# Kernel optimization log

Measured on AMD Instinct MI355X. Metric: run time of the kernel, lower is better.

Reference implementation:

```python
import jax, jax.numpy as jnp
import numpy as np

N, E, E_LBL = 50000, 800000, 200000
D_IN, H = 128, 128


def setup_inputs() -> dict:
    key = jax.random.key(0)
    ks = jax.random.split(key, 12)
    s = 0.05
    return {
        "x": jax.random.normal(ks[0], (N, D_IN), jnp.float32),
        "edge_index": jax.random.randint(ks[1], (2, E), 0, N, jnp.int64),
        "edge_label_index": jax.random.randint(ks[2], (2, E_LBL), 0, N, jnp.int64),
        "pre_w": jax.random.normal(ks[3], (D_IN, H), jnp.float32) * s,
        "pre_b": jax.random.normal(ks[4], (H,), jnp.float32) * s,
        "Wx": jax.random.normal(ks[5], (3, 2, H, H), jnp.float32) * s,  # gates z,r,h x cheb orders T0,T1
        "bx": jax.random.normal(ks[6], (3, H), jnp.float32) * s,
        "Wh": jax.random.normal(ks[7], (3, 2, H, H), jnp.float32) * s,
        "bh": jax.random.normal(ks[8], (3, H), jnp.float32) * s,
        "post_w": jax.random.normal(ks[9], (H, 2), jnp.float32) * s,
        "post_b": jax.random.normal(ks[10], (2,), jnp.float32) * s,
    }


def reference(x, edge_index, edge_label_index, pre_w, pre_b, Wx, bx, Wh, bh, post_w, post_b):
    n = x.shape[0]
    src, dst = edge_index[0], edge_index[1]

    # Scaled Chebyshev Laplacian (sym norm, lambda_max=2): L_hat = -D^{-1/2} A D^{-1/2}
    # (diagonal of L_hat is exactly 0, so only off-diagonal edge terms remain).
    deg = jax.ops.segment_sum(jnp.ones_like(src, dtype=x.dtype), src, num_segments=n)
    dinv = jnp.where(deg > 0, jax.lax.rsqrt(jnp.maximum(deg, 1.0)), 0.0)
    w = -(dinv[src] * dinv[dst])  # [E]

    def lap(v):  # L_hat @ v : gather src rows, weight, scatter-add at dst
        return jax.ops.segment_sum(w[:, None] * v[src], dst, num_segments=n)

    def cheb(v, Lv, W2, b):  # ChebConv K=2: T0(v)@W0 + T1(v)@W1 + b
        return v @ W2[0] + Lv @ W2[1] + b

    # pre: Linear(input_dim -> hidden)
    Xh = x @ pre_w + pre_b  # [N, H]
    LX = lap(Xh)

    # GConvGRU single step, H0 = 0
    Hc = jnp.zeros_like(Xh)
    LH = lap(Hc)
    Z = jax.nn.sigmoid(cheb(Xh, LX, Wx[0], bx[0]) + cheb(Hc, LH, Wh[0], bh[0]))
    R = jax.nn.sigmoid(cheb(Xh, LX, Wx[1], bx[1]) + cheb(Hc, LH, Wh[1], bh[1]))
    HR = Hc * R
    LHR = lap(HR)
    Ht = jnp.tanh(cheb(Xh, LX, Wx[2], bx[2]) + cheb(HR, LHR, Wh[2], bh[2]))
    Hc = Z * Hc + (1.0 - Z) * Ht

    h = jax.nn.relu(Hc)
    # link decoder: gather endpoints, hadamard, Linear(H->2), sum over logits
    hprod = h[edge_label_index[0]] * h[edge_label_index[1]]  # [E_lbl, H]
    out = hprod @ post_w + post_b  # [E_lbl, 2]
    return jnp.sum(out, axis=-1)  # [E_lbl]
```

## Files before the change

kernel.cpp:

```cpp
#include <hip/hip_runtime.h>
#include <math.h>


#define RND 2048
#define SORT_CAP 1536
#define CAPB 6144

typedef __attribute__((ext_vector_type(4))) float f32x4;
typedef __attribute__((ext_vector_type(8))) short short8;
typedef __attribute__((ext_vector_type(4))) unsigned u32x4;

static __device__ __forceinline__ unsigned short f2b(float f) {
  union { float f; unsigned u; } v; v.f = f;
  unsigned r = (v.u + 0x7fffu + ((v.u >> 16) & 1u)) >> 16;
  return (unsigned short)r;
}
static __device__ __forceinline__ float b2f(unsigned short s) {
  union { unsigned u; float f; } v; v.u = ((unsigned)s) << 16;
  return v.f;
}

__global__ __launch_bounds__(256) void prep_kernel(const float* __restrict__ pre_w, const float* __restrict__ Wx,
                                                   const float* __restrict__ bx, const float* __restrict__ bh,
                                                   const float* __restrict__ post_w, const float* __restrict__ post_b,
                                                   unsigned short* __restrict__ Bt1c, unsigned short* __restrict__ Btc2,
                                                   float* __restrict__ fb2, float* __restrict__ pwsum,
                                                   int* __restrict__ binPos) {
  int e = blockIdx.x * 256 + threadIdx.x;
  if (e < 512) binPos[e] = (e & 255) * CAPB;
  if (e < 16384) {
    int kc = e >> 12, r = e & 4095, col = r >> 5, kk = r & 31;
    Bt1c[e] = f2b(pre_w[(kc * 32 + kk) * 128 + col]);
  }
  int e2 = e - 16384;
  if (e2 >= 0 && e2 < 65536) {
    int kc = e2 >> 13, r = e2 & 8191, cB = r >> 5, kk = r & 31;
    int k = kc * 32 + kk, half = k >> 7, ki = k & 127;
    int cb = cB >> 7, r7 = cB & 127, nw6 = r7 >> 6, u2 = r7 & 63;
    int g = (u2 >= 32) ? 2 : 0, hcol = cb * 64 + nw6 * 32 + (u2 & 31);
    Btc2[e2] = f2b(Wx[((g * 2 + half) * 128 + ki) * 128 + hcol]);
  }
  int e3 = e - (16384 + 65536);
  if (e3 >= 0 && e3 < 256) {
    int cB = e3;
    int cb = cB >> 7, r7 = cB & 127, nw6 = r7 >> 6, u2 = r7 & 63;
    int g = (u2 >= 32) ? 2 : 0, hcol = cb * 64 + nw6 * 32 + (u2 & 31);
    fb2[cB] = bx[g * 128 + hcol] + bh[g * 128 + hcol];
  }
  int e4 = e - (16384 + 65536 + 256);
  if (e4 >= 0 && e4 < 128) pwsum[e4] = post_w[2 * e4] + post_w[2 * e4 + 1];
  if (e4 == 128) pwsum[128] = post_b[0] + post_b[1];
}

union SMemU {
  struct { unsigned short As[128 * 40]; unsigned short Bs[128 * 40]; } g;
  struct { unsigned ent[RND]; int hist[256], lstart[256], lofs[256], gbase[256], wsum[4];
           unsigned char ebin[RND], sb[RND]; } s;
};

__global__ __launch_bounds__(256) void mega1_kernel(const float* __restrict__ x,
                                                    const unsigned short* __restrict__ Bt1c,
                                                    const float* __restrict__ pre_b,
                                                    unsigned short* __restrict__ Xq,
                                                    const int* __restrict__ ei, int* __restrict__ binPos,
                                                    unsigned* __restrict__ bins,
                                                    unsigned char* __restrict__ sbins,
                                                    int N, int E, int RB) {
  __shared__ SMemU sm;
  const int t = threadIdx.x;

  if ((int)blockIdx.x < RB) {
    unsigned short* As = sm.g.As;
    unsigned short* Bs = sm.g.Bs;
    const int r0 = blockIdx.x * 128;
    const int w = t >> 6, lane = t & 63;
    const int m = lane & 15, q = lane >> 4;
    const int mw = (w >> 1) * 64, nw = (w & 1) * 64;

    f32x4 acc[4][4];
#pragma unroll
    for (int i = 0; i < 4; ++i)
#pragma unroll
      for (int j = 0; j < 4; ++j) acc[i][j] = {0.f, 0.f, 0.f, 0.f};

    const int arow = t >> 1, aseg = t & 1;
    const bool arow_ok = (r0 + arow) < N;
    const float* asrc0 = &x[(size_t)(r0 + arow) * 128 + aseg * 16];

    float4 cav[4]; short8 cbv0, cbv1;
    {
      if (arow_ok) {
#pragma unroll
        for (int i = 0; i < 4; ++i) cav[i] = *(const float4*)(asrc0 + i * 4);
      } else {
#pragma unroll
        for (int i = 0; i < 4; ++i) cav[i] = make_float4(0.f, 0.f, 0.f, 0.f);
      }
      const char* src = (const char*)Bt1c + t * 32;
      cbv0 = *(const short8*)src;
      cbv1 = *(const short8*)(src + 16);
    }

    for (int kc = 0; kc < 4; ++kc) {
      __syncthreads();
      {
        short8 t0, t1;
#pragma unroll
        for (int i = 0; i < 2; ++i) {
          t0[i * 4 + 0] = (short)f2b(cav[i].x); t0[i * 4 + 1] = (short)f2b(cav[i].y);
          t0[i * 4 + 2] = (short)f2b(cav[i].z); t0[i * 4 + 3] = (short)f2b(cav[i].w);
          t1[i * 4 + 0] = (short)f2b(cav[i + 2].x); t1[i * 4 + 1] = (short)f2b(cav[i + 2].y);
          t1[i * 4 + 2] = (short)f2b(cav[i + 2].z); t1[i * 4 + 3] = (short)f2b(cav[i + 2].w);
        }
        *(short8*)&As[arow * 40 + aseg * 16] = t0;
        *(short8*)&As[arow * 40 + aseg * 16 + 8] = t1;
        int bcol = t >> 1, boff = (t & 1) * 16;
        *(short8*)&Bs[bcol * 40 + boff] = cbv0;
        *(short8*)&Bs[bcol * 40 + boff + 8] = cbv1;
      }
      float4 nav[4]; short8 nbv0, nbv1;
      if (kc < 3) {
        if (arow_ok) {
          const float* src = asrc0 + (kc + 1) * 32;
#pragma unroll
          for (int i = 0; i < 4; ++i) nav[i] = *(const float4*)(src + i * 4);
        } else {
#pragma unroll
          for (int i = 0; i < 4; ++i) nav[i] = make_float4(0.f, 0.f, 0.f, 0.f);
        }
        const char* src = (const char*)Bt1c + (size_t)(kc + 1) * 8192 + t * 32;
        nbv0 = *(const short8*)src;
        nbv1 = *(const short8*)(src + 16);
      }
      __syncthreads();
      short8 af[4], bf[4];
#pragma unroll
      for (int i = 0; i < 4; ++i) af[i] = *(const short8*)&As[(mw + i * 16 + m) * 40 + q * 8];
#pragma unroll
      for (int j = 0; j < 4; ++j) bf[j] = *(const short8*)&Bs[(nw + j * 16 + m) * 40 + q * 8];
#pragma unroll
      for (int i = 0; i < 4; ++i)
#pragma unroll
        for (int j = 0; j < 4; ++j)
          acc[i][j] = __builtin_amdgcn_mfma_f32_16x16x32_bf16(af[i], bf[j], acc[i][j], 0, 0, 0);
      if (kc < 3) {
#pragma unroll
        for (int i = 0; i < 4; ++i) cav[i] = nav[i];
        cbv0 = nbv0; cbv1 = nbv1;
      }
    }

#pragma unroll
    for (int i = 0; i < 4; ++i) {
      int rb2 = r0 + mw + i * 16 + q * 4;
#pragma unroll
      for (int j = 0; j < 4; ++j) {
        int col = nw + j * 16 + m;
        float bias = pre_b[col];
#pragma unroll
        for (int r = 0; r < 4; ++r) {
          int row = rb2 + r;
          if (row < N) Xq[(size_t)row * 128 + col] = f2b(acc[i][j][r] + bias);
        }
      }
    }
    return;
  }

  unsigned* ent = sm.s.ent;
  unsigned char* ebin = sm.s.ebin;
  unsigned char* sb = sm.s.sb;
  int* hist = sm.s.hist;
  int* lstart = sm.s.lstart;
  int* lofs = sm.s.lofs;
  int* gbase = sm.s.gbase;
  int* wsum = sm.s.wsum;
  const int sbid = (int)blockIdx.x - RB;
  const int snum = (int)gridDim.x - RB;
  const int w = t >> 6, lane = t & 63;
  for (long long base = (long long)sbid * RND; base < E; base += (long long)snum * RND) {
    int cnt = (int)(((long long)E - base < RND) ? (E - base) : RND);
    if (t < 256) hist[t] = 0;
    __syncthreads();
    int my_s[8], my_d[8];
#pragma unroll
    for (int u = 0; u < 8; ++u) {
      int i = u * 256 + t;
      my_s[u] = -1;
      if (i < cnt) {
        int idx = (int)base + i;
        my_s[u] = ei[idx];
        my_d[u] = ei[E + idx];
        atomicAdd(&hist[my_d[u] >> 8], 1);
      }
    }
    __syncthreads();
    {
      int h = hist[t];
      hist[t] = 0;
      int v = h;
#pragma unroll
      for (int dd = 1; dd < 64; dd <<= 1) { int uu = __shfl_up(v, dd); if (lane >= dd) v += uu; }
      if (lane == 63) wsum[w] = v;
      __syncthreads();
      int woff = 0;
#pragma unroll
      for (int ww = 0; ww < 3; ++ww) if (ww < w) woff += wsum[ww];
      int excl = v - h + woff;
      lstart[t] = excl; lofs[t] = excl;
      if (h > 0) gbase[t] = atomicAdd(&binPos[t], h);
    }
    __syncthreads();
#pragma unroll
    for (int u = 0; u < 8; ++u) {
      if (my_s[u] >= 0) {
        int b = my_d[u] >> 8;
        int p = atomicAdd(&lofs[b], 1);
        ent[p] = (unsigned)my_s[u] | ((unsigned)(my_d[u] & 255) << 16);
        ebin[p] = (unsigned char)b;
        atomicAdd(&hist[my_s[u] >> 8], 1);
      }
    }
    __syncthreads();
    for (int i = t; i < cnt; i += 256) {
      int b = ebin[i];
      int pos = gbase[b] + (i - lstart[b]);
      if (pos < (b + 1) * CAPB) bins[pos] = ent[i];
    }
    __syncthreads();
    {
      int h = hist[t];
      int v = h;
#pragma unroll
      for (int dd = 1; dd < 64; dd <<= 1) { int uu = __shfl_up(v, dd); if (lane >= dd) v += uu; }
      if (lane == 63) wsum[w] = v;
      __syncthreads();
      int woff = 0;
#pragma unroll
      for (int ww = 0; ww < 3; ++ww) if (ww < w) woff += wsum[ww];
      int excl = v - h + woff;
      lstart[t] = excl; lofs[t] = excl;
      if (h > 0) gbase[t] = atomicAdd(&binPos[256 + t], h);
    }
    __syncthreads();
#pragma unroll
    for (int u = 0; u < 8; ++u) {
      if (my_s[u] >= 0) {
        int b = my_s[u] >> 8;
        int p = atomicAdd(&lofs[b], 1);
        sb[p] = (unsigned char)(my_s[u] & 255);
        ebin[p] = (unsigned char)b;
      }
    }
    __syncthreads();
    for (int i = t; i < cnt; i += 256) {
      int b = ebin[i];
      int pos = gbase[b] + (i - lstart[b]);
      if (pos < (b + 1) * CAPB) sbins[pos] = sb[i];
    }
    __syncthreads();
  }
}

__global__ __launch_bounds__(512) void deghist_kernel(const unsigned char* __restrict__ sbins,
                                                      const int* __restrict__ binPos,
                                                      const unsigned short* __restrict__ Xq,
                                                      unsigned short* __restrict__ Xs,
                                                      float* __restrict__ dinvNeg, int N) {
  __shared__ int h[256];
  __shared__ float sdi[256];
  const int t = threadIdx.x;
  const int bin = blockIdx.x;
  if (t < 256) h[t] = 0;
  __syncthreads();
  int T2 = binPos[256 + bin] - bin * CAPB;
  if (T2 > CAPB) T2 = CAPB;
  const unsigned char* __restrict__ p = sbins + (size_t)bin * CAPB;
  for (int i = t; i < T2; i += 512) atomicAdd(&h[p[i]], 1);
  __syncthreads();
  if (t < 256) {
    int node = bin * 256 + t;
    float di = h[t] > 0 ? rsqrtf((float)h[t]) : 0.0f;
    sdi[t] = di;
    if (node < N) dinvNeg[node] = -di;
  }
  __syncthreads();
  const int wv = t >> 6, lane = t & 63;
  const int g4 = lane >> 4, sl = lane & 15;
#pragma unroll
  for (int it = 0; it < 8; ++it) {
    int r = wv * 32 + it * 4 + g4;
    int rnode = bin * 256 + r;
    if (rnode < N) {
      float di_r = sdi[r];
      u32x4 v = *(const u32x4*)((const char*)Xq + (size_t)rnode * 256 + sl * 16);
      u32x4 o;
#pragma unroll
      for (int k = 0; k < 4; ++k) {
        union { unsigned u32; float f; } fl, fh;
        fl.u32 = v[k] << 16; fh.u32 = v[k] & 0xffff0000u;
        o[k] = (unsigned)f2b(fl.f * di_r) | ((unsigned)f2b(fh.f * di_r) << 16);
      }
      *(u32x4*)((char*)Xs + (size_t)rnode * 256 + sl * 16) = o;
    }
  }
}

__global__ __launch_bounds__(512) void lap_bin_kernel(const unsigned short* __restrict__ Xs,
                                                      unsigned short* __restrict__ LXc,
                                                      const unsigned* __restrict__ bins,
                                                      const int* __restrict__ binPos,
                                                      const float* __restrict__ dinvNeg, int N) {
  __shared__ unsigned eLDS[CAPB];
  __shared__ unsigned short sortS[SORT_CAP];
  __shared__ int hist[64], start[64], off[64];
  const int t = threadIdx.x;
  const int bin = blockIdx.x >> 2, qt = blockIdx.x & 3;
  const int lo = bin * CAPB;
  int T = binPos[bin] - lo;
  if (T > CAPB) T = CAPB;
  const unsigned* __restrict__ ebase = &bins[lo];
  if (t < 64) hist[t] = 0;
  __syncthreads();
  for (int i = t; i < T; i += 512) {
    unsigned e = ebase[i];
    eLDS[i] = e;
    int dl = (e >> 16) & 255;
    if ((dl >> 6) == qt) atomicAdd(&hist[dl & 63], 1);
  }
  __syncthreads();
  if (t < 64) {
    int h = hist[t];
    int v = h;
#pragma unroll
    for (int d = 1; d < 64; d <<= 1) {
      int u = __shfl_up(v, d);
      if (t >= d) v += u;
    }
    start[t] = v - h;
    off[t] = v - h;
  }
  __syncthreads();
  for (int i = t; i < T; i += 512) {
    unsigned e = eLDS[i];
    int dl = (e >> 16) & 255;
    if ((dl >> 6) == qt) {
      int p = atomicAdd(&off[dl & 63], 1);
      if (p < SORT_CAP) sortS[p] = (unsigned short)(e & 0xFFFFu);
    }
  }
  __syncthreads();
  const int wv = t >> 6, lane = t & 63;
  const int g4 = lane >> 4, sl = lane & 15;
  for (int n = wv; n < 64; n += 8) {
    int node = bin * 256 + qt * 64 + n;
    if (node >= N) break;
    int st = start[n], cnum = hist[n];
    float acc[8] = {0.f, 0.f, 0.f, 0.f, 0.f, 0.f, 0.f, 0.f};
    for (int j = 0; j < cnum; j += 8) {
#pragma unroll
      for (int u = 0; u < 2; ++u) {
        int idx = j + u * 4 + g4;
        bool val = idx < cnum;
        int s = sortS[st + (val ? idx : 0)];
        u32x4 vv = *(const u32x4*)((const char*)Xs + (size_t)s * 256 + sl * 16);
        if (val) {
#pragma unroll
          for (int k = 0; k < 4; ++k) {
            union { unsigned u32; float f; } fl, fh;
            fl.u32 = vv[k] << 16; fh.u32 = vv[k] & 0xffff0000u;
            acc[2 * k] += fl.f;
            acc[2 * k + 1] += fh.f;
          }
        }
      }
    }
#pragma unroll
    for (int k = 0; k < 8; ++k) {
      acc[k] += __shfl_xor(acc[k], 16);
      acc[k] += __shfl_xor(acc[k], 32);
    }
    if (g4 == 0) {
      float wd = dinvNeg[node];
      u32x4 o;
#pragma unroll
      for (int k = 0; k < 4; ++k)
        o[k] = (unsigned)f2b(acc[2 * k] * wd) | ((unsigned)f2b(acc[2 * k + 1] * wd) << 16);
      *(u32x4*)((char*)LXc + (size_t)node * 256 + sl * 16) = o;
    }
  }
}

__global__ __launch_bounds__(256) void gemm2_mfma(const unsigned short* __restrict__ Xq,
                                                  const unsigned short* __restrict__ LXc,
                                                  const unsigned short* __restrict__ Btc2,
                                                  const float* __restrict__ fb2,
                                                  unsigned short* __restrict__ hb, int N) {
  __shared__ unsigned short As[128 * 40];
  __shared__ unsigned short Bs[128 * 40];
  const int t = threadIdx.x;
  const int rb = blockIdx.x >> 1, cb = blockIdx.x & 1;
  const int r0 = rb * 128;
  const int w = t >> 6, lane = t & 63;
  const int m = lane & 15, q = lane >> 4;
  const int mw = (w >> 1) * 64, nw = (w & 1) * 64;

  f32x4 acc[4][4];
#pragma unroll
  for (int i = 0; i < 4; ++i)
#pragma unroll
    for (int j = 0; j < 4; ++j) acc[i][j] = {0.f, 0.f, 0.f, 0.f};

  const int arow = t >> 1;
  const int aoff = (t & 1) * 32;
  const char* aXq = (const char*)Xq + (size_t)(r0 + arow) * 256 + aoff;
  const char* aLX = (const char*)LXc + (size_t)(r0 + arow) * 256 + aoff;
  const char* bsrc0 = (const char*)Btc2 + (size_t)cb * 8192 + t * 32;

  short8 cav0, cav1, cbv0, cbv1;
  cav0 = *(const short8*)aXq;
  cav1 = *(const short8*)(aXq + 16);
  cbv0 = *(const short8*)bsrc0;
  cbv1 = *(const short8*)(bsrc0 + 16);

  for (int kc = 0; kc < 8; ++kc) {
    __syncthreads();
    *(short8*)&As[arow * 40 + (aoff >> 1)] = cav0;
    *(short8*)&As[arow * 40 + (aoff >> 1) + 8] = cav1;
    {
      int bcol = t >> 1, boff = (t & 1) * 16;
      *(short8*)&Bs[bcol * 40 + boff] = cbv0;
      *(short8*)&Bs[bcol * 40 + boff + 8] = cbv1;
    }
    short8 nav0, nav1, nbv0, nbv1;
    if (kc < 7) {
      int kn = kc + 1;
      const char* asrc = (kn < 4) ? (aXq + kn * 64) : (aLX + (kn - 4) * 64);
      nav0 = *(const short8*)asrc;
      nav1 = *(const short8*)(asrc + 16);
      const char* bsrc = bsrc0 + (size_t)kn * 16384;
      nbv0 = *(const short8*)bsrc;
      nbv1 = *(const short8*)(bsrc + 16);
    }
    __syncthreads();
    short8 af[4], bf[4];
#pragma unroll
    for (int i = 0; i < 4; ++i) af[i] = *(const short8*)&As[(mw + i * 16 + m) * 40 + q * 8];
#pragma unroll
    for (int j = 0; j < 4; ++j) bf[j] = *(const short8*)&Bs[(nw + j * 16 + m) * 40 + q * 8];
#pragma unroll
    for (int i = 0; i < 4; ++i)
#pragma unroll
      for (int j = 0; j < 4; ++j)
        acc[i][j] = __builtin_amdgcn_mfma_f32_16x16x32_bf16(af[i], bf[j], acc[i][j], 0, 0, 0);
    if (kc < 7) { cav0 = nav0; cav1 = nav1; cbv0 = nbv0; cbv1 = nbv1; }
  }

#pragma unroll
  for (int i = 0; i < 4; ++i) {
    int rbase = r0 + mw + i * 16 + q * 4;
#pragma unroll
    for (int jz = 0; jz < 2; ++jz) {
      int cBz = cb * 128 + nw + jz * 16 + m;
      int hc = cb * 64 + (nw >> 1) + jz * 16 + m;
      float bz = fb2[cBz], bt = fb2[cBz + 32];
#pragma unroll
      for (int r = 0; r < 4; ++r) {
        int row = rbase + r;
        if (row < N) {
          float zp = acc[i][jz][r] + bz;
          float tp = acc[i][jz + 2][r] + bt;
          float zs = 1.0f / (1.0f + __expf(-zp));
          float th = tanhf(tp);
          hb[(size_t)row * 128 + hc] = f2b(fmaxf((1.0f - zs) * th, 0.0f));
        }
      }
    }
  }
}

__global__ __launch_bounds__(256) void decoder_kernel(const unsigned short* __restrict__ hb,
                                                      const int* __restrict__ eli,
                                                      const float* __restrict__ pwsum, float* __restrict__ out, int M) {
  int t = threadIdx.x;
  int i = blockIdx.x * 16 + (t >> 4);
  int l = t & 15;
  if (i >= M) return;
  int a = eli[i], b = eli[M + i];
  int k = l * 8;
  short8 va = *(const short8*)&hb[(size_t)a * 128 + k];
  short8 vb = *(const short8*)&hb[(size_t)b * 128 + k];
  const float4* pwp = (const float4*)&pwsum[k];
  float4 p0 = pwp[0], p1 = pwp[1];
  float s = 0.0f;
  s += b2f((unsigned short)va[0]) * b2f((unsigned short)vb[0]) * p0.x;
  s += b2f((unsigned short)va[1]) * b2f((unsigned short)vb[1]) * p0.y;
  s += b2f((unsigned short)va[2]) * b2f((unsigned short)vb[2]) * p0.z;
  s += b2f((unsigned short)va[3]) * b2f((unsigned short)vb[3]) * p0.w;
  s += b2f((unsigned short)va[4]) * b2f((unsigned short)vb[4]) * p1.x;
  s += b2f((unsigned short)va[5]) * b2f((unsigned short)vb[5]) * p1.y;
  s += b2f((unsigned short)va[6]) * b2f((unsigned short)vb[6]) * p1.z;
  s += b2f((unsigned short)va[7]) * b2f((unsigned short)vb[7]) * p1.w;
#pragma unroll
  for (int off = 8; off; off >>= 1) s += __shfl_xor(s, off);
  if (l == 0) out[i] = s + pwsum[128];
}

extern "C" void kernel_launch(void* const* d_in, const int* in_sizes, int n_in,
                              void* d_out, int out_size, void* d_ws, size_t ws_size,
                              hipStream_t stream) {
  const float* x      = (const float*)d_in[0];
  const int*   ei     = (const int*)d_in[1];
  const int*   eli    = (const int*)d_in[2];
  const float* pre_w  = (const float*)d_in[3];
  const float* pre_b  = (const float*)d_in[4];
  const float* Wx     = (const float*)d_in[5];
  const float* bx     = (const float*)d_in[6];
  const float* bh     = (const float*)d_in[8];
  const float* post_w = (const float*)d_in[9];
  const float* post_b = (const float*)d_in[10];
  float* out = (float*)d_out;

  const int N = in_sizes[0] / 128;
  const int E = in_sizes[1] / 2;
  const int M = in_sizes[2] / 2;
  const int RB = (N + 127) / 128;
  const int NBIN = (N + 255) / 256;
  const int SCAT = (E + RND - 1) / RND;

  char* W = (char*)d_ws;
  size_t o = 0;
  float* dinvNeg = (float*)(W + o); o += (size_t)N * 4;
  int* binPos = (int*)(W + o);    o += 2048;
  o = (o + 255) & ~(size_t)255;
  unsigned* bins = (unsigned*)(W + o); o += (size_t)NBIN * CAPB * 4;
  o = (o + 255) & ~(size_t)255;
  unsigned char* sbins = (unsigned char*)(W + o); o += (size_t)NBIN * CAPB;
  o = (o + 255) & ~(size_t)255;
  unsigned short* Xq = (unsigned short*)(W + o);  o += (size_t)RB * 128 * 256;
  unsigned short* Xs = (unsigned short*)(W + o);  o += (size_t)RB * 128 * 256;
  unsigned short* LXc = (unsigned short*)(W + o); o += (size_t)RB * 128 * 256;
  unsigned short* hb = (unsigned short*)(W + o);  o += (size_t)N * 256;
  unsigned short* Bt1c = (unsigned short*)(W + o); o += 32768;
  unsigned short* Btc2 = (unsigned short*)(W + o); o += 131072;
  float* fb2 = (float*)(W + o);  o += 1024;
  float* pwsum = (float*)(W + o); o += 768;

  prep_kernel<<<322, 256, 0, stream>>>(pre_w, Wx, bx, bh, post_w, post_b, Bt1c, Btc2, fb2, pwsum,
                                       binPos);
  mega1_kernel<<<RB + SCAT, 256, 0, stream>>>(x, Bt1c, pre_b, Xq, ei, binPos, bins, sbins, N, E, RB);
  deghist_kernel<<<NBIN, 512, 0, stream>>>(sbins, binPos, Xq, Xs, dinvNeg, N);
  lap_bin_kernel<<<NBIN * 4, 512, 0, stream>>>(Xs, LXc, bins, binPos, dinvNeg, N);
  gemm2_mfma<<<RB * 2, 256, 0, stream>>>(Xq, LXc, Btc2, fb2, hb, N);
  decoder_kernel<<<(M + 15) / 16, 256, 0, stream>>>(hb, eli, pwsum, out, M);
}
```

Baseline: 197.5 us.

## Store scaled features in FP8 E4M3 for Laplacian gather and pad bin counters

```diff
diff --git a/kernel.cpp b/kernel.cpp
--- a/kernel.cpp
+++ b/kernel.cpp
@@ -9,6 +9,7 @@
 typedef __attribute__((ext_vector_type(4))) float f32x4;
 typedef __attribute__((ext_vector_type(8))) short short8;
 typedef __attribute__((ext_vector_type(4))) unsigned u32x4;
+typedef __attribute__((ext_vector_type(2))) unsigned u32x2;
 
 static __device__ __forceinline__ unsigned short f2b(float f) {
   union { float f; unsigned u; } v; v.f = f;
@@ -18,6 +19,17 @@
 static __device__ __forceinline__ float b2f(unsigned short s) {
   union { unsigned u; float f; } v; v.u = ((unsigned)s) << 16;
   return v.f;
+}
+static __device__ __forceinline__ unsigned f2e4m3(float f) {
+  unsigned su = (__float_as_uint(f) >> 24) & 0x80u;
+  float a = fminf(fabsf(f), 448.0f) * 0x1.0p-120f;
+  unsigned u = __float_as_uint(a);
+  u += 0x7FFFFu + ((u >> 20) & 1u);
+  return su | ((u >> 20) & 0x7Fu);
+}
+static __device__ __forceinline__ float e4m32f(unsigned b) {
+  unsigned u = ((b & 0x80u) << 24) | ((b & 0x7Fu) << 20);
+  return __uint_as_float(u) * 0x1.0p120f;
 }
 
 __global__ __launch_bounds__(256) void prep_kernel(const float* __restrict__ pre_w, const float* __restrict__ Wx,
@@ -27,7 +39,7 @@
                                                    float* __restrict__ fb2, float* __restrict__ pwsum,
                                                    int* __restrict__ binPos) {
   int e = blockIdx.x * 256 + threadIdx.x;
-  if (e < 512) binPos[e] = (e & 255) * CAPB;
+  if (e < 512) binPos[e * 16] = (e & 255) * CAPB;
   if (e < 16384) {
     int kc = e >> 12, r = e & 4095, col = r >> 5, kk = r & 31;
     Bt1c[e] = f2b(pre_w[(kc * 32 + kk) * 128 + col]);
@@ -208,7 +220,7 @@
       for (int ww = 0; ww < 3; ++ww) if (ww < w) woff += wsum[ww];
       int excl = v - h + woff;
       lstart[t] = excl; lofs[t] = excl;
-      if (h > 0) gbase[t] = atomicAdd(&binPos[t], h);
+      if (h > 0) gbase[t] = atomicAdd(&binPos[t * 16], h);
     }
     __syncthreads();
 #pragma unroll
@@ -240,7 +252,7 @@
       for (int ww = 0; ww < 3; ++ww) if (ww < w) woff += wsum[ww];
       int excl = v - h + woff;
       lstart[t] = excl; lofs[t] = excl;
-      if (h > 0) gbase[t] = atomicAdd(&binPos[256 + t], h);
+      if (h > 0) gbase[t] = atomicAdd(&binPos[(256 + t) * 16], h);
     }
     __syncthreads();
 #pragma unroll
@@ -265,7 +277,7 @@
 __global__ __launch_bounds__(512) void deghist_kernel(const unsigned char* __restrict__ sbins,
                                                       const int* __restrict__ binPos,
                                                       const unsigned short* __restrict__ Xq,
-                                                      unsigned short* __restrict__ Xs,
+                                                      unsigned char* __restrict__ Xs,
                                                       float* __restrict__ dinvNeg, int N) {
   __shared__ int h[256];
   __shared__ float sdi[256];
@@ -273,7 +285,7 @@
   const int bin = blockIdx.x;
   if (t < 256) h[t] = 0;
   __syncthreads();
-  int T2 = binPos[256 + bin] - bin * CAPB;
+  int T2 = binPos[(256 + bin) * 16] - bin * CAPB;
   if (T2 > CAPB) T2 = CAPB;
   const unsigned char* __restrict__ p = sbins + (size_t)bin * CAPB;
   for (int i = t; i < T2; i += 512) atomicAdd(&h[p[i]], 1);
@@ -294,19 +306,26 @@
     if (rnode < N) {
       float di_r = sdi[r];
       u32x4 v = *(const u32x4*)((const char*)Xq + (size_t)rnode * 256 + sl * 16);
-      u32x4 o;
-#pragma unroll
-      for (int k = 0; k < 4; ++k) {
-        union { unsigned u32; float f; } fl, fh;
-        fl.u32 = v[k] << 16; fh.u32 = v[k] & 0xffff0000u;
-        o[k] = (unsigned)f2b(fl.f * di_r) | ((unsigned)f2b(fh.f * di_r) << 16);
-      }
-      *(u32x4*)((char*)Xs + (size_t)rnode * 256 + sl * 16) = o;
-    }
-  }
-}
-
-__global__ __launch_bounds__(512) void lap_bin_kernel(const unsigned short* __restrict__ Xs,
+      u32x2 o;
+#pragma unroll
+      for (int k = 0; k < 2; ++k) {
+        unsigned w0 = 0;
+#pragma unroll
+        for (int j = 0; j < 2; ++j) {
+          unsigned vv = v[k * 2 + j];
+          union { unsigned u32; float f; } fl, fh;
+          fl.u32 = vv << 16; fh.u32 = vv & 0xffff0000u;
+          w0 |= f2e4m3(fl.f * di_r) << (j * 16);
+          w0 |= f2e4m3(fh.f * di_r) << (j * 16 + 8);
+        }
+        o[k] = w0;
+      }
+      *(u32x2*)((char*)Xs + (size_t)rnode * 128 + sl * 8) = o;
+    }
+  }
+}
+
+__global__ __launch_bounds__(512) void lap_bin_kernel(const unsigned char* __restrict__ Xs,
                                                       unsigned short* __restrict__ LXc,
                                                       const unsigned* __restrict__ bins,
                                                       const int* __restrict__ binPos,
@@ -317,7 +336,7 @@
   const int t = threadIdx.x;
   const int bin = blockIdx.x >> 2, qt = blockIdx.x & 3;
   const int lo = bin * CAPB;
-  int T = binPos[bin] - lo;
+  int T = binPos[bin * 16] - lo;
   if (T > CAPB) T = CAPB;
   const unsigned* __restrict__ ebase = &bins[lo];
   if (t < 64) hist[t] = 0;
@@ -363,14 +382,15 @@
         int idx = j + u * 4 + g4;
         bool val = idx < cnum;
         int s = sortS[st + (val ? idx : 0)];
-        u32x4 vv = *(const u32x4*)((const char*)Xs + (size_t)s * 256 + sl * 16);
+        u32x2 vv = *(const u32x2*)((const char*)Xs + (size_t)s * 128 + sl * 8);
         if (val) {
 #pragma unroll
-          for (int k = 0; k < 4; ++k) {
-            union { unsigned u32; float f; } fl, fh;
-            fl.u32 = vv[k] << 16; fh.u32 = vv[k] & 0xffff0000u;
-            acc[2 * k] += fl.f;
-            acc[2 * k + 1] += fh.f;
+          for (int kk = 0; kk < 2; ++kk) {
+            unsigned wv2 = vv[kk];
+            acc[4 * kk + 0] += e4m32f(wv2 & 0xFFu);
+            acc[4 * kk + 1] += e4m32f((wv2 >> 8) & 0xFFu);
+            acc[4 * kk + 2] += e4m32f((wv2 >> 16) & 0xFFu);
+            acc[4 * kk + 3] += e4m32f(wv2 >> 24);
           }
         }
       }
@@ -531,14 +551,15 @@
   char* W = (char*)d_ws;
   size_t o = 0;
   float* dinvNeg = (float*)(W + o); o += (size_t)N * 4;
-  int* binPos = (int*)(W + o);    o += 2048;
+  o = (o + 255) & ~(size_t)255;
+  int* binPos = (int*)(W + o);    o += 512 * 16 * 4;
   o = (o + 255) & ~(size_t)255;
   unsigned* bins = (unsigned*)(W + o); o += (size_t)NBIN * CAPB * 4;
   o = (o + 255) & ~(size_t)255;
   unsigned char* sbins = (unsigned char*)(W + o); o += (size_t)NBIN * CAPB;
   o = (o + 255) & ~(size_t)255;
   unsigned short* Xq = (unsigned short*)(W + o);  o += (size_t)RB * 128 * 256;
-  unsigned short* Xs = (unsigned short*)(W + o);  o += (size_t)RB * 128 * 256;
+  unsigned char* Xs = (unsigned char*)(W + o);    o += (size_t)RB * 128 * 128;
   unsigned short* LXc = (unsigned short*)(W + o); o += (size_t)RB * 128 * 256;
   unsigned short* hb = (unsigned short*)(W + o);  o += (size_t)N * 256;
   unsigned short* Bt1c = (unsigned short*)(W + o); o += 32768;
```

After: 216.6 us. 1.1x slower.

## Pad bin counters, vectorize edge loads, pack bin id, split lap bins finer

Applied to the files above, without the earlier changes.

```diff
diff --git a/kernel.cpp b/kernel.cpp
--- a/kernel.cpp
+++ b/kernel.cpp
@@ -9,6 +9,7 @@
 typedef __attribute__((ext_vector_type(4))) float f32x4;
 typedef __attribute__((ext_vector_type(8))) short short8;
 typedef __attribute__((ext_vector_type(4))) unsigned u32x4;
+typedef __attribute__((ext_vector_type(4))) int i32x4;
 
 static __device__ __forceinline__ unsigned short f2b(float f) {
   union { float f; unsigned u; } v; v.f = f;
@@ -27,7 +28,7 @@
                                                    float* __restrict__ fb2, float* __restrict__ pwsum,
                                                    int* __restrict__ binPos) {
   int e = blockIdx.x * 256 + threadIdx.x;
-  if (e < 512) binPos[e] = (e & 255) * CAPB;
+  if (e < 512) binPos[e * 16] = (e & 255) * CAPB;
   if (e < 16384) {
     int kc = e >> 12, r = e & 4095, col = r >> 5, kk = r & 31;
     Bt1c[e] = f2b(pre_w[(kc * 32 + kk) * 128 + col]);
@@ -183,16 +184,27 @@
     if (t < 256) hist[t] = 0;
     __syncthreads();
     int my_s[8], my_d[8];
-#pragma unroll
-    for (int u = 0; u < 8; ++u) {
-      int i = u * 256 + t;
-      my_s[u] = -1;
-      if (i < cnt) {
-        int idx = (int)base + i;
-        my_s[u] = ei[idx];
-        my_d[u] = ei[E + idx];
-        atomicAdd(&hist[my_d[u] >> 8], 1);
-      }
+    {
+      long long e0 = base + (long long)t * 8;
+      if (e0 + 8 <= E && 8 * t + 8 <= cnt) {
+        const i32x4* ps = (const i32x4*)&ei[e0];
+        const i32x4* pd = (const i32x4*)&ei[E + e0];
+        i32x4 s0 = ps[0], s1 = ps[1], d0 = pd[0], d1 = pd[1];
+#pragma unroll
+        for (int u = 0; u < 4; ++u) { my_s[u] = s0[u]; my_d[u] = d0[u]; }
+#pragma unroll
+        for (int u = 0; u < 4; ++u) { my_s[4 + u] = s1[u]; my_d[4 + u] = d1[u]; }
+      } else {
+#pragma unroll
+        for (int u = 0; u < 8; ++u) {
+          int i = t * 8 + u;
+          my_s[u] = -1;
+          if (i < cnt) { my_s[u] = ei[base + i]; my_d[u] = ei[E + base + i]; }
+        }
+      }
+#pragma unroll
+      for (int u = 0; u < 8; ++u)
+        if (my_s[u] >= 0) atomicAdd(&hist[my_d[u] >> 8], 1);
     }
     __syncthreads();
     {
@@ -208,7 +220,7 @@
       for (int ww = 0; ww < 3; ++ww) if (ww < w) woff += wsum[ww];
       int excl = v - h + woff;
       lstart[t] = excl; lofs[t] = excl;
-      if (h > 0) gbase[t] = atomicAdd(&binPos[t], h);
+      if (h > 0) gbase[t] = atomicAdd(&binPos[t * 16], h);
     }
     __syncthreads();
 #pragma unroll
@@ -216,16 +228,16 @@
       if (my_s[u] >= 0) {
         int b = my_d[u] >> 8;
         int p = atomicAdd(&lofs[b], 1);
-        ent[p] = (unsigned)my_s[u] | ((unsigned)(my_d[u] & 255) << 16);
-        ebin[p] = (unsigned char)b;
+        ent[p] = (unsigned)my_s[u] | ((unsigned)(my_d[u] & 255) << 16) | ((unsigned)b << 24);
         atomicAdd(&hist[my_s[u] >> 8], 1);
       }
     }
     __syncthreads();
     for (int i = t; i < cnt; i += 256) {
-      int b = ebin[i];
+      unsigned e = ent[i];
+      int b = e >> 24;
       int pos = gbase[b] + (i - lstart[b]);
-      if (pos < (b + 1) * CAPB) bins[pos] = ent[i];
+      if (pos < (b + 1) * CAPB) bins[pos] = e;
     }
     __syncthreads();
     {
@@ -240,7 +252,7 @@
       for (int ww = 0; ww < 3; ++ww) if (ww < w) woff += wsum[ww];
       int excl = v - h + woff;
       lstart[t] = excl; lofs[t] = excl;
-      if (h > 0) gbase[t] = atomicAdd(&binPos[256 + t], h);
+      if (h > 0) gbase[t] = atomicAdd(&binPos[(256 + t) * 16], h);
     }
     __syncthreads();
 #pragma unroll
@@ -273,7 +285,7 @@
   const int bin = blockIdx.x;
   if (t < 256) h[t] = 0;
   __syncthreads();
-  int T2 = binPos[256 + bin] - bin * CAPB;
+  int T2 = binPos[(256 + bin) * 16] - bin * CAPB;
   if (T2 > CAPB) T2 = CAPB;
   const unsigned char* __restrict__ p = sbins + (size_t)bin * CAPB;
   for (int i = t; i < T2; i += 512) atomicAdd(&h[p[i]], 1);
@@ -313,27 +325,27 @@
                                                       const float* __restrict__ dinvNeg, int N) {
   __shared__ unsigned eLDS[CAPB];
   __shared__ unsigned short sortS[SORT_CAP];
-  __shared__ int hist[64], start[64], off[64];
+  __shared__ int hist[32], start[32], off[32];
   const int t = threadIdx.x;
-  const int bin = blockIdx.x >> 2, qt = blockIdx.x & 3;
+  const int bin = blockIdx.x >> 3, qt = blockIdx.x & 7;
   const int lo = bin * CAPB;
-  int T = binPos[bin] - lo;
+  int T = binPos[bin * 16] - lo;
   if (T > CAPB) T = CAPB;
   const unsigned* __restrict__ ebase = &bins[lo];
-  if (t < 64) hist[t] = 0;
+  if (t < 32) hist[t] = 0;
   __syncthreads();
   for (int i = t; i < T; i += 512) {
     unsigned e = ebase[i];
     eLDS[i] = e;
     int dl = (e >> 16) & 255;
-    if ((dl >> 6) == qt) atomicAdd(&hist[dl & 63], 1);
-  }
-  __syncthreads();
-  if (t < 64) {
+    if ((dl >> 5) == qt) atomicAdd(&hist[dl & 31], 1);
+  }
+  __syncthreads();
+  if (t < 32) {
     int h = hist[t];
     int v = h;
 #pragma unroll
-    for (int d = 1; d < 64; d <<= 1) {
+    for (int d = 1; d < 32; d <<= 1) {
       int u = __shfl_up(v, d);
       if (t >= d) v += u;
     }
@@ -344,16 +356,16 @@
   for (int i = t; i < T; i += 512) {
     unsigned e = eLDS[i];
     int dl = (e >> 16) & 255;
-    if ((dl >> 6) == qt) {
-      int p = atomicAdd(&off[dl & 63], 1);
+    if ((dl >> 5) == qt) {
+      int p = atomicAdd(&off[dl & 31], 1);
       if (p < SORT_CAP) sortS[p] = (unsigned short)(e & 0xFFFFu);
     }
   }
   __syncthreads();
   const int wv = t >> 6, lane = t & 63;
   const int g4 = lane >> 4, sl = lane & 15;
-  for (int n = wv; n < 64; n += 8) {
-    int node = bin * 256 + qt * 64 + n;
+  for (int n = wv; n < 32; n += 8) {
+    int node = bin * 256 + qt * 32 + n;
     if (node >= N) break;
     int st = start[n], cnum = hist[n];
     float acc[8] = {0.f, 0.f, 0.f, 0.f, 0.f, 0.f, 0.f, 0.f};
@@ -531,7 +543,8 @@
   char* W = (char*)d_ws;
   size_t o = 0;
   float* dinvNeg = (float*)(W + o); o += (size_t)N * 4;
-  int* binPos = (int*)(W + o);    o += 2048;
+  o = (o + 255) & ~(size_t)255;
+  int* binPos = (int*)(W + o);    o += 512 * 16 * 4;
   o = (o + 255) & ~(size_t)255;
   unsigned* bins = (unsigned*)(W + o); o += (size_t)NBIN * CAPB * 4;
   o = (o + 255) & ~(size_t)255;
@@ -550,7 +563,7 @@
                                        binPos);
   mega1_kernel<<<RB + SCAT, 256, 0, stream>>>(x, Bt1c, pre_b, Xq, ei, binPos, bins, sbins, N, E, RB);
   deghist_kernel<<<NBIN, 512, 0, stream>>>(sbins, binPos, Xq, Xs, dinvNeg, N);
-  lap_bin_kernel<<<NBIN * 4, 512, 0, stream>>>(Xs, LXc, bins, binPos, dinvNeg, N);
+  lap_bin_kernel<<<NBIN * 8, 512, 0, stream>>>(Xs, LXc, bins, binPos, dinvNeg, N);
   gemm2_mfma<<<RB * 2, 256, 0, stream>>>(Xq, LXc, Btc2, fb2, hb, N);
   decoder_kernel<<<(M + 15) / 16, 256, 0, stream>>>(hb, eli, pwsum, out, M);
 }
```

Measured after the change: 200.9 us. Within noise of the previous version (+1.8%).
